# Performance work log

Hardware: AMD Instinct MI355X
Metric: run time of the kernel (lower is better)

Reference implementation:

```python
import jax, jax.numpy as jnp
import numpy as np

B, N, DIN, DE, NH, DK = 4, 256, 128, 64, 8, 16


def setup_inputs() -> dict:
    key = jax.random.key(0)
    ks = jax.random.split(key, 8)
    s = 0.05
    return {
        "h": jax.random.normal(ks[0], (B, N, DIN), jnp.float32),
        "e": jax.random.normal(ks[1], (B, N, N, DE), jnp.float32),
        "mask": jnp.ones((B, N), jnp.float32),
        "WQ": jax.random.normal(ks[2], (DIN, NH * DK), jnp.float32) * s,
        "WK": jax.random.normal(ks[3], (DIN, NH * DK), jnp.float32) * s,
        "WV": jax.random.normal(ks[4], (DIN, NH * DK), jnp.float32) * s,
        "WE": jax.random.normal(ks[5], (DE, NH * DK), jnp.float32) * s,
        "WE2": jax.random.normal(ks[6], (DE, NH * DK), jnp.float32) * s,
    }


def reference(h, e, mask, WQ, WK, WV, WE, WE2):
    b, n, _ = h.shape
    Q = (h @ WQ).reshape(b, n, NH, DK)
    K = (h @ WK).reshape(b, n, NH, DK) * (float(DK) ** -0.5)
    V = (h @ WV).reshape(b, n, NH, DK)
    E = (e @ WE).reshape(b, n, n, NH, DK)
    E2 = (e @ WE2).reshape(b, n, n, NH, DK)
    # edge-augmented scores: (b, i, j, h, k)
    scores = jnp.einsum('bihk,bjhk->bijh', Q, K)[..., None] + E2
    scores = jnp.exp(jnp.clip(scores, -5.0, 5.0))
    attn_mask = mask[:, :, None, None, None] * mask[:, None, :, None, None]
    scores = scores * attn_mask
    softmax_denom = jnp.clip(scores.sum(axis=2), 1e-6, None)  # (b,i,h,k)
    scores = scores * attn_mask  # attn_dropout p=0.0 -> identity
    out = jnp.einsum('bijhk,bjhk->bihk', scores, V)
    out = out + (scores * E).sum(axis=2)
    out = out / softmax_denom
    return out.reshape(b, n, NH * DK)
```

## Files before the change

### kernel.cpp

```cpp
#include <hip/hip_runtime.h>

#define BB   4
#define NN   256
#define DIN  128
#define DE   64
#define NH   8
#define DK   16
#define CC   128

typedef __attribute__((ext_vector_type(8))) short short8;
typedef __attribute__((ext_vector_type(4))) float f32x4;

__device__ __forceinline__ unsigned short f2bfu(float f) {
    union { float f; unsigned int i; } v; v.f = f;
    unsigned int x = v.i;
    x += 0x7FFFu + ((x >> 16) & 1u);
    return (unsigned short)(x >> 16);
}

__global__ __launch_bounds__(256) void qkv_kernel(
    const float* __restrict__ h, const float* __restrict__ WQ,
    const float* __restrict__ WK, const float* __restrict__ WV,
    const float* __restrict__ WE, const float* __restrict__ WE2,
    float* __restrict__ Qw, float* __restrict__ Kw, float* __restrict__ Vt,
    unsigned short* __restrict__ wfrag)
{
    const int t = threadIdx.x;

    if (blockIdx.x >= 256) {
        const int tid  = (blockIdx.x - 256) * 256 + t;
        const int m    = tid >> 10;
        const int g    = (tid >> 7) & 7;
        const int ks   = (tid >> 6) & 1;
        const int lane = tid & 63;
        const int q4 = lane >> 4, l15 = lane & 15;
        const float* W = m ? WE2 : WE;
        union { uint4 u; unsigned short s[8]; } pk;
        #pragma unroll
        for (int ii = 0; ii < 8; ++ii) {
            const int d = ks * 32 + q4 * 8 + ii;
            pk.s[ii] = f2bfu(W[d * CC + g * 16 + l15]);
        }
        ((uint4*)wfrag)[tid] = pk.u;
        return;
    }

    __shared__ float hsh[4 * DIN];
    __shared__ float psum[4 * 1536];
    const int r0 = blockIdx.x * 4;

    hsh[t]       = h[(size_t)r0 * DIN + t];
    hsh[256 + t] = h[(size_t)r0 * DIN + 256 + t];
    __syncthreads();

    const int cp  = t & 63;
    const int qtr = t >> 6;
    float aq[4][2], ak[4][2], av[4][2];
    #pragma unroll
    for (int r = 0; r < 4; ++r)
        aq[r][0]=aq[r][1]=ak[r][0]=ak[r][1]=av[r][0]=av[r][1]=0.f;

    #pragma unroll 4
    for (int dd = 0; dd < 32; ++dd) {
        const int d = qtr * 32 + dd;
        const float2 fq = ((const float2*)WQ)[d * 64 + cp];
        const float2 fk = ((const float2*)WK)[d * 64 + cp];
        const float2 fv = ((const float2*)WV)[d * 64 + cp];
        #pragma unroll
        for (int r = 0; r < 4; ++r) {
            const float hd = hsh[r * DIN + d];
            aq[r][0] = fmaf(hd, fq.x, aq[r][0]); aq[r][1] = fmaf(hd, fq.y, aq[r][1]);
            ak[r][0] = fmaf(hd, fk.x, ak[r][0]); ak[r][1] = fmaf(hd, fk.y, ak[r][1]);
            av[r][0] = fmaf(hd, fv.x, av[r][0]); av[r][1] = fmaf(hd, fv.y, av[r][1]);
        }
    }
    float* pq = psum + qtr * 1536;
    #pragma unroll
    for (int r = 0; r < 4; ++r) {
        pq[r*384       + 2*cp] = aq[r][0]; pq[r*384       + 2*cp+1] = aq[r][1];
        pq[r*384 + 128 + 2*cp] = ak[r][0]; pq[r*384 + 128 + 2*cp+1] = ak[r][1];
        pq[r*384 + 256 + 2*cp] = av[r][0]; pq[r*384 + 256 + 2*cp+1] = av[r][1];
    }
    __syncthreads();

    const int b  = r0 >> 8;
    const int j0 = r0 & 255;
    #pragma unroll
    for (int k = 0; k < 6; ++k) {
        const int o = k * 256 + t;
        float v = psum[o] + psum[1536 + o] + psum[3072 + o] + psum[4608 + o];
        const int r   = o / 384;
        const int mc  = o - r * 384;
        const int mat = mc >> 7;
        const int c   = mc & 127;
        if      (mat == 0) Qw[(size_t)(r0 + r) * CC + c] = v;
        else if (mat == 1) Kw[(size_t)(r0 + r) * CC + c] = v * 0.25f;
        else               Vt[((size_t)(b * CC) + c) * NN + j0 + r] = v;
    }
}

__global__ __launch_bounds__(256, 5) void attn_kernel(
    const float* __restrict__ e, const float* __restrict__ maskp,
    const unsigned short* __restrict__ wfrag,
    const float* __restrict__ Qw, const float* __restrict__ Kw,
    const float* __restrict__ Vt, float* __restrict__ out)
{
    __shared__ __align__(16) unsigned short esh[128 * DE];
    __shared__ float qk_sh[NH * NN];
    __shared__ float msk_sh[NN];
    __shared__ float qrow_sh[CC];

    const int row  = blockIdx.x;
    const int b    = row >> 8, i = row & 255;
    const int t    = threadIdx.x;
    const int wave = t >> 6, lane = t & 63;
    const int q4   = lane >> 4;
    const int l15  = lane & 15;

    const float4* esrc = (const float4*)(e + (size_t)row * NN * DE);
    uint4* edst = (uint4*)esh;

    short8 bfrag[2][2][2];
    {
        const uint4* wf = (const uint4*)wfrag;
        #pragma unroll
        for (int m = 0; m < 2; ++m)
        #pragma unroll
        for (int ct = 0; ct < 2; ++ct) {
            const int g = wave * 2 + ct;
            #pragma unroll
            for (int ks = 0; ks < 2; ++ks) {
                union { uint4 u; short8 s8; } cv;
                cv.u = wf[((m * 8 + g) * 2 + ks) * 64 + lane];
                bfrag[m][ct][ks] = cv.s8;
            }
        }
    }

    if (t < CC) qrow_sh[t] = Qw[(size_t)row * CC + t];
    msk_sh[t] = maskp[b * NN + t];

    #pragma unroll
    for (int r = 0; r < 4; ++r) {
        const int cidx = r * 256 + t;
        const int j = cidx >> 3, ch = cidx & 7;
        const float4 f0 = esrc[2 * cidx];
        const float4 f1 = esrc[2 * cidx + 1];
        union { uint4 u; unsigned short s[8]; } pk;
        pk.s[0]=f2bfu(f0.x); pk.s[1]=f2bfu(f0.y); pk.s[2]=f2bfu(f0.z); pk.s[3]=f2bfu(f0.w);
        pk.s[4]=f2bfu(f1.x); pk.s[5]=f2bfu(f1.y); pk.s[6]=f2bfu(f1.z); pk.s[7]=f2bfu(f1.w);
        edst[j * 8 + (ch ^ (j & 7))] = pk.u;
    }
    __syncthreads();

    {
        const float4* kr = (const float4*)(Kw + (size_t)(b * NN + t) * CC);
        #pragma unroll
        for (int hh = 0; hh < NH; ++hh) {
            float s = 0.f;
            #pragma unroll
            for (int p = 0; p < 4; ++p) {
                const float4 kv = kr[hh * 4 + p];
                const int qb = hh * 16 + p * 4;
                s += kv.x * qrow_sh[qb]     + kv.y * qrow_sh[qb + 1]
                   + kv.z * qrow_sh[qb + 2] + kv.w * qrow_sh[qb + 3];
            }
            qk_sh[hh * 256 + t] = s;
        }
    }
    __syncthreads();

    const float mi = msk_sh[i];
    float acc[2] = {0.f, 0.f}, dnm[2] = {0.f, 0.f};
    const short8* ep = (const short8*)esh;

    #pragma unroll
    for (int hf = 0; hf < 2; ++hf) {
        if (hf == 1) {
            __syncthreads();
            #pragma unroll
            for (int r = 0; r < 4; ++r) {
                const int cidx = r * 256 + t;
                const int j = cidx >> 3, ch = cidx & 7;
                const float4 f0 = esrc[2048 + 2 * cidx];
                const float4 f1 = esrc[2048 + 2 * cidx + 1];
                union { uint4 u; unsigned short s[8]; } pk;
                pk.s[0]=f2bfu(f0.x); pk.s[1]=f2bfu(f0.y); pk.s[2]=f2bfu(f0.z); pk.s[3]=f2bfu(f0.w);
                pk.s[4]=f2bfu(f1.x); pk.s[5]=f2bfu(f1.y); pk.s[6]=f2bfu(f1.z); pk.s[7]=f2bfu(f1.w);
                edst[j * 8 + (ch ^ (j & 7))] = pk.u;
            }
            __syncthreads();
        }
        #pragma unroll 2
        for (int s = 0; s < 8; ++s) {
            const int ja = s * 16 + l15;
            const short8 a0 = ep[ja * 8 + ((q4    ) ^ (ja & 7))];
            const short8 a1 = ep[ja * 8 + ((q4 + 4) ^ (ja & 7))];
            #pragma unroll
            for (int ct = 0; ct < 2; ++ct) {
                const int g = wave * 2 + ct;
                f32x4 s2 = {0.f,0.f,0.f,0.f}, eE = {0.f,0.f,0.f,0.f};
                s2 = __builtin_amdgcn_mfma_f32_16x16x32_bf16(a0, bfrag[1][ct][0], s2, 0,0,0);
                s2 = __builtin_amdgcn_mfma_f32_16x16x32_bf16(a1, bfrag[1][ct][1], s2, 0,0,0);
                eE = __builtin_amdgcn_mfma_f32_16x16x32_bf16(a0, bfrag[0][ct][0], eE, 0,0,0);
                eE = __builtin_amdgcn_mfma_f32_16x16x32_bf16(a1, bfrag[0][ct][1], eE, 0,0,0);
                const int j0 = hf * 128 + s * 16 + q4 * 4;
                union { float4 v; float a[4]; } v4;
                v4.v = *(const float4*)
                    (Vt + ((size_t)(b * CC) + g * 16 + l15) * NN + j0);
                #pragma unroll
                for (int r = 0; r < 4; ++r) {
                    const int jr = j0 + r;
                    float sc = qk_sh[g * 256 + jr] + s2[r];
                    sc = fminf(5.f, fmaxf(-5.f, sc));
                    const float p  = __expf(sc);
                    const float mm = mi * msk_sh[jr];
                    const float s1 = p * mm;
                    dnm[ct] += s1;
                    acc[ct] = fmaf(s1 * mm, v4.a[r] + eE[r], acc[ct]);
                }
            }
        }
    }

    #pragma unroll
    for (int ct = 0; ct < 2; ++ct) {
        float a = acc[ct], d = dnm[ct];
        a += __shfl_xor(a, 16); a += __shfl_xor(a, 32);
        d += __shfl_xor(d, 16); d += __shfl_xor(d, 32);
        acc[ct] = a; dnm[ct] = d;
    }
    if (lane < 32) {
        const int ct = lane >> 4;
        out[(size_t)row * CC + wave * 32 + lane] = acc[ct] / fmaxf(dnm[ct], 1e-6f);
    }
}

extern "C" void kernel_launch(void* const* d_in, const int* in_sizes, int n_in,
                              void* d_out, int out_size, void* d_ws, size_t ws_size,
                              hipStream_t stream)
{
    const float* h    = (const float*)d_in[0];
    const float* e    = (const float*)d_in[1];
    const float* mask = (const float*)d_in[2];
    const float* WQ   = (const float*)d_in[3];
    const float* WK   = (const float*)d_in[4];
    const float* WV   = (const float*)d_in[5];
    const float* WE   = (const float*)d_in[6];
    const float* WE2  = (const float*)d_in[7];

    unsigned short* wfrag = (unsigned short*)d_ws;
    float* Qw = (float*)((char*)d_ws + 32768);
    float* Kw = Qw + BB * NN * CC;
    float* Vt = Kw + BB * NN * CC;

    qkv_kernel <<<264,   256, 0, stream>>>(h, WQ, WK, WV, WE, WE2,
                                           Qw, Kw, Vt, wfrag);
    attn_kernel<<<BB*NN, 256, 0, stream>>>(e, mask, wfrag, Qw, Kw, Vt,
                                           (float*)d_out);
}
```

Before: 148.1 us.

## Prefetch second half of edge tile into registers and vectorize LDS reads

The global loads for the second 128-row half of the edge tile are now issued before the first barrier and held in registers, so their latency overlaps the QK dot products and the first half's MFMA loop. The loads of qk scores and mask values from shared memory become float4 reads, replacing scalar reads. The occupancy hint of 5 blocks in the launch bounds is removed because the prefetch buffer adds 32 VGPRs per thread, which may lower occupancy or cause spills.

```diff
diff --git a/kernel.cpp b/kernel.cpp
--- a/kernel.cpp
+++ b/kernel.cpp
@@ -99,16 +99,16 @@
     }
 }
 
-__global__ __launch_bounds__(256, 5) void attn_kernel(
+__global__ __launch_bounds__(256) void attn_kernel(
     const float* __restrict__ e, const float* __restrict__ maskp,
     const unsigned short* __restrict__ wfrag,
     const float* __restrict__ Qw, const float* __restrict__ Kw,
     const float* __restrict__ Vt, float* __restrict__ out)
 {
     __shared__ __align__(16) unsigned short esh[128 * DE];
-    __shared__ float qk_sh[NH * NN];
-    __shared__ float msk_sh[NN];
-    __shared__ float qrow_sh[CC];
+    __shared__ __align__(16) float qk_sh[NH * NN];
+    __shared__ __align__(16) float msk_sh[NN];
+    __shared__ __align__(16) float qrow_sh[CC];
 
     const int row  = blockIdx.x;
     const int b    = row >> 8, i = row & 255;
@@ -151,6 +151,15 @@
         pk.s[4]=f2bfu(f1.x); pk.s[5]=f2bfu(f1.y); pk.s[6]=f2bfu(f1.z); pk.s[7]=f2bfu(f1.w);
         edst[j * 8 + (ch ^ (j & 7))] = pk.u;
     }
+
+    float4 pf[8];
+    #pragma unroll
+    for (int r = 0; r < 4; ++r) {
+        const int cidx = r * 256 + t;
+        pf[2*r]     = esrc[2048 + 2 * cidx];
+        pf[2*r + 1] = esrc[2048 + 2 * cidx + 1];
+    }
+
     __syncthreads();
 
     {
@@ -182,8 +191,8 @@
             for (int r = 0; r < 4; ++r) {
                 const int cidx = r * 256 + t;
                 const int j = cidx >> 3, ch = cidx & 7;
-                const float4 f0 = esrc[2048 + 2 * cidx];
-                const float4 f1 = esrc[2048 + 2 * cidx + 1];
+                const float4 f0 = pf[2 * r];
+                const float4 f1 = pf[2 * r + 1];
                 union { uint4 u; unsigned short s[8]; } pk;
                 pk.s[0]=f2bfu(f0.x); pk.s[1]=f2bfu(f0.y); pk.s[2]=f2bfu(f0.z); pk.s[3]=f2bfu(f0.w);
                 pk.s[4]=f2bfu(f1.x); pk.s[5]=f2bfu(f1.y); pk.s[6]=f2bfu(f1.z); pk.s[7]=f2bfu(f1.w);
@@ -196,6 +205,9 @@
             const int ja = s * 16 + l15;
             const short8 a0 = ep[ja * 8 + ((q4    ) ^ (ja & 7))];
             const short8 a1 = ep[ja * 8 + ((q4 + 4) ^ (ja & 7))];
+            const int j0g = hf * 128 + s * 16 + q4 * 4;
+            union { float4 v; float a[4]; } mk4;
+            mk4.v = *(const float4*)(msk_sh + j0g);
             #pragma unroll
             for (int ct = 0; ct < 2; ++ct) {
                 const int g = wave * 2 + ct;
@@ -204,17 +216,15 @@
                 s2 = __builtin_amdgcn_mfma_f32_16x16x32_bf16(a1, bfrag[1][ct][1], s2, 0,0,0);
                 eE = __builtin_amdgcn_mfma_f32_16x16x32_bf16(a0, bfrag[0][ct][0], eE, 0,0,0);
                 eE = __builtin_amdgcn_mfma_f32_16x16x32_bf16(a1, bfrag[0][ct][1], eE, 0,0,0);
-                const int j0 = hf * 128 + s * 16 + q4 * 4;
-                union { float4 v; float a[4]; } v4;
-                v4.v = *(const float4*)
-                    (Vt + ((size_t)(b * CC) + g * 16 + l15) * NN + j0);
+                union { float4 v; float a[4]; } v4, qk4;
+                v4.v  = *(const float4*)(Vt + ((size_t)(b * CC) + g * 16 + l15) * NN + j0g);
+                qk4.v = *(const float4*)(qk_sh + g * 256 + j0g);
                 #pragma unroll
                 for (int r = 0; r < 4; ++r) {
-                    const int jr = j0 + r;
-                    float sc = qk_sh[g * 256 + jr] + s2[r];
+                    float sc = qk4.a[r] + s2[r];
                     sc = fminf(5.f, fmaxf(-5.f, sc));
                     const float p  = __expf(sc);
-                    const float mm = mi * msk_sh[jr];
+                    const float mm = mi * mk4.a[r];
                     const float s1 = p * mm;
                     dnm[ct] += s1;
                     acc[ct] = fmaf(s1 * mm, v4.a[r] + eE[r], acc[ct]);
```

After: 143.4 us. 3.1% less time.
